# Optimization experiments

Measured on AMD Instinct MI355X. Metric: run time of the kernel, lower is better.

## Reference

```python
import jax, jax.numpy as jnp
import numpy as np

N = 500_000
E = 5_000_000
DIM = 16
LR = 0.005
THRESHOLD = 0.0


def setup_inputs() -> dict:
    key = jax.random.key(0)
    ks = jax.random.split(key, 8)
    s = 1.0 / np.sqrt(DIM)
    return {
        "x": jax.random.normal(ks[0], (N, DIM), jnp.float32),
        "edge_index": jax.random.randint(ks[1], (2, E), 0, N, dtype=jnp.int32),
        "W1": jax.random.normal(ks[2], (DIM, DIM), jnp.float32) * s,
        "b1": jnp.zeros((DIM,), jnp.float32),
        "W2": jax.random.normal(ks[3], (DIM, DIM), jnp.float32) * s,
        "b2": jnp.zeros((DIM,), jnp.float32),
        "W3": jax.random.normal(ks[4], (DIM, DIM), jnp.float32) * s,
        "b3": jnp.zeros((DIM,), jnp.float32),
        "positive": 0,  # negative sample -> nonzero loss branch
    }


def gcn_conv(x, edge_index, W, b):
    # PyG GCNConv: h = x @ W.T, add self-loops, symmetric norm, aggregate at dst.
    n = x.shape[0]
    loop = jnp.arange(n, dtype=edge_index.dtype)
    src = jnp.concatenate([edge_index[0], loop])
    dst = jnp.concatenate([edge_index[1], loop])
    deg = jax.ops.segment_sum(jnp.ones_like(dst, x.dtype), dst, num_segments=n)
    dinv = jnp.where(deg > 0, jax.lax.rsqrt(deg), 0.0)
    norm = dinv[src] * dinv[dst]  # [E+N]
    h = x @ W.T  # [N, out]
    msg = norm[:, None] * h[src]  # irregular gather, memory-bound
    return jax.ops.segment_sum(msg, dst, num_segments=n) + b


def local_loss(g, positive):
    t = THRESHOLD
    if positive:
        return jnp.where(g > t + 10.0, 0.0,
               jnp.where(g < t - 10.0, t - g, jnp.log1p(jnp.exp(t - g))))
    return jnp.where(g > t + 10.0, t + g,
           jnp.where(g < t - 10.0, 0.0, jnp.log1p(jnp.exp(g + t))))


def reference(x, edge_index, W1, b1, W2, b2, W3, b3, positive):
    # Note: the original computes activation_normalizer(x) and loss_derivative(g)
    # into z/driv_loss but immediately overwrites both -> dead code, omitted.
    agg = jnp.float32(0.0)
    Wc, bc = W1, b1  # conv1 params, updated in-place each layer in the original
    x_cur = x
    for (W, b) in ((W1, b1), (W2, b2), (W3, b3)):
        z = jax.nn.relu(gcn_conv(x_cur, edge_index, W, b))
        goodness = jnp.sum(z * z) / z.shape[1]
        agg = agg + local_loss(goodness, positive)
        d = 2.0 * jnp.abs(z)            # activation_gradient(z)
        wd = d * d                      # weighted_deriv
        dW = x_cur.T @ wd               # [in, out]
        db = jnp.sum(wd, axis=0)
        Wc = Wc - LR * dW.T
        bc = bc - LR * db
        x_cur = z
    return agg, Wc, bc
```

## Files before the change

### kernel.cpp

```cpp
#include <hip/hip_runtime.h>
#include <math.h>

#define TPB 256
#define TPB_P 512
#define TPB_A 512
#define LRATE 0.005f

#define LOG_NPB 10
#define NPB (1 << LOG_NPB)
#define CAP 14336

#define LOG_SUP 13
#define NS1 64
#define CAP1 90112
#define NS2 8
#define CHUNK 4096
#define CPT (CHUNK / TPB_P)

#define NTILE 64

#define FXS  65536.0f
#define FXSI (1.0f / 65536.0f)

#if __has_builtin(__builtin_amdgcn_cvt_f32_fp8) && __has_builtin(__builtin_amdgcn_cvt_pk_fp8_f32)
__device__ __forceinline__ float fp8_dec(unsigned char v) {
    return __builtin_amdgcn_cvt_f32_fp8((int)v, 0);
}
__device__ __forceinline__ unsigned fp8_pk4(float a, float b, float c, float d) {
    int w = __builtin_amdgcn_cvt_pk_fp8_f32(a, b, 0, false);
    w = __builtin_amdgcn_cvt_pk_fp8_f32(c, d, w, true);
    return (unsigned)w;
}
#else
__device__ __forceinline__ unsigned char fp8_enc1(float f) {
    unsigned u = __float_as_uint(f);
    unsigned s = (u >> 24) & 0x80u;
    u &= 0x7FFFFFFFu;
    if (u >= 0x43E00000u) return (unsigned char)(s | 0x7E);
    if (u < 0x3C800000u) {
        float a = __uint_as_float(u);
        int m = (int)rintf(a * 512.f);
        return (unsigned char)(s | (unsigned)m);
    }
    unsigned mant = u & 0x7FFFFFu;
    unsigned rest = mant & 0xFFFFFu;
    unsigned keep = u >> 20;
    keep += (rest > 0x80000u || (rest == 0x80000u && (keep & 1u))) ? 1u : 0u;
    int eb = (int)(keep >> 3) - 127 + 7;
    return (unsigned char)(s | (unsigned)((eb << 3) | (int)(keep & 7u)));
}
__device__ __forceinline__ float fp8_dec(unsigned char v) {
    unsigned s = ((unsigned)(v & 0x80u)) << 24;
    unsigned e = (v >> 3) & 0xFu;
    unsigned m = v & 7u;
    if (e == 0) {
        float r = (float)m * 0.001953125f;
        return (v & 0x80u) ? -r : r;
    }
    return __uint_as_float(s | ((e + 120u) << 23) | (m << 20));
}
__device__ __forceinline__ unsigned fp8_pk4(float a, float b, float c, float d) {
    return (unsigned)fp8_enc1(a) | ((unsigned)fp8_enc1(b) << 8) |
           ((unsigned)fp8_enc1(c) << 16) | ((unsigned)fp8_enc1(d) << 24);
}
#endif

#if __has_builtin(__builtin_amdgcn_cvt_pk_f32_fp8)
typedef float __attribute__((ext_vector_type(2))) f32x2;
__device__ __forceinline__ void fp8_dec4(unsigned w, float& a, float& b, float& c, float& d) {
    f32x2 lo = __builtin_amdgcn_cvt_pk_f32_fp8((int)w, false);
    f32x2 hi = __builtin_amdgcn_cvt_pk_f32_fp8((int)w, true);
    a = lo[0]; b = lo[1]; c = hi[0]; d = hi[1];
}
#else
__device__ __forceinline__ void fp8_dec4(unsigned w, float& a, float& b, float& c, float& d) {
    a = fp8_dec((unsigned char)(w & 0xFFu));
    b = fp8_dec((unsigned char)((w >> 8) & 0xFFu));
    c = fp8_dec((unsigned char)((w >> 16) & 0xFFu));
    d = fp8_dec((unsigned char)((w >> 24) & 0xFFu));
}
#endif

__global__ __launch_bounds__(TPB_P) void k_part1(const int* __restrict__ src,
                                                 const int* __restrict__ dst,
                                                 int* __restrict__ bcur1,
                                                 int* __restrict__ grec1,
                                                 int E) {
    __shared__ int hist[NS1], lstart[NS1], lcur[NS1], gbase[NS1];
    __shared__ int lbuf[CHUNK];
    __shared__ unsigned char bbuf[CHUNK];
    int t = threadIdx.x;
    int chunkBase = blockIdx.x * CHUNK;
    if (t < NS1) hist[t] = 0;
    __syncthreads();

    int myb[CPT], myrec[CPT];
#pragma unroll
    for (int k = 0; k < CPT; k++) {
        int e = chunkBase + k * TPB_P + t;
        if (e < E) {
            int d = dst[e];
            int s = src[e];
            myb[k] = d >> LOG_SUP;
            myrec[k] = (s << LOG_SUP) | (d & ((1 << LOG_SUP) - 1));
            atomicAdd(&hist[myb[k]], 1);
        } else myb[k] = -1;
    }
    __syncthreads();
    if (t == 0) {
        int run = 0;
        for (int k2 = 0; k2 < NS1; k2++) {
            int c = hist[k2]; lstart[k2] = run; lcur[k2] = run; run += c;
        }
    }
    __syncthreads();
    if (t < NS1 && hist[t] > 0) gbase[t] = atomicAdd(&bcur1[t * 16], hist[t]);
    __syncthreads();
#pragma unroll
    for (int k = 0; k < CPT; k++) {
        if (myb[k] >= 0) {
            int p = atomicAdd(&lcur[myb[k]], 1);
            lbuf[p] = myrec[k];
            bbuf[p] = (unsigned char)myb[k];
        }
    }
    __syncthreads();
    int total = E - chunkBase; if (total > CHUNK) total = CHUNK;
    for (int p = t; p < total; p += TPB_P) {
        int b = (int)bbuf[p];
        int pos = gbase[b] + (p - lstart[b]);
        if (pos < CAP1) grec1[(size_t)b * CAP1 + pos] = lbuf[p];
    }
}

__global__ __launch_bounds__(TPB_P) void k_part2(const int* __restrict__ bcur1,
                                                 const int* __restrict__ grec1,
                                                 int* __restrict__ bcur,
                                                 int* __restrict__ grec) {
    __shared__ int hist[NS2], lstart[NS2], lcur[NS2], gbase[NS2];
    __shared__ int lbuf[CHUNK];
    __shared__ unsigned char bbuf[CHUNK];
    int t = threadIdx.x;
    int s = blockIdx.x;
    int cnt1 = bcur1[s * 16]; if (cnt1 > CAP1) cnt1 = CAP1;
    int chunkBase = blockIdx.y * CHUNK;
    if (chunkBase >= cnt1) return;
    int total = cnt1 - chunkBase; if (total > CHUNK) total = CHUNK;
    if (t < NS2) hist[t] = 0;
    __syncthreads();

    int myb[CPT], myrec[CPT];
#pragma unroll
    for (int k = 0; k < CPT; k++) {
        int i = chunkBase + k * TPB_P + t;
        if (i < cnt1) {
            int r = grec1[(size_t)s * CAP1 + i];
            int sub = (r >> LOG_NPB) & (NS2 - 1);
            myb[k] = sub;
            myrec[k] = (int)((((unsigned)r) >> LOG_SUP) << LOG_NPB) | (r & (NPB - 1));
            atomicAdd(&hist[sub], 1);
        } else myb[k] = -1;
    }
    __syncthreads();
    if (t == 0) {
        int run = 0;
        for (int k2 = 0; k2 < NS2; k2++) {
            int c = hist[k2]; lstart[k2] = run; lcur[k2] = run; run += c;
        }
    }
    __syncthreads();
    if (t < NS2 && hist[t] > 0) gbase[t] = atomicAdd(&bcur[(s * NS2 + t) * 16], hist[t]);
    __syncthreads();
#pragma unroll
    for (int k = 0; k < CPT; k++) {
        if (myb[k] >= 0) {
            int p = atomicAdd(&lcur[myb[k]], 1);
            lbuf[p] = myrec[k];
            bbuf[p] = (unsigned char)myb[k];
        }
    }
    __syncthreads();
    for (int p = t; p < total; p += TPB_P) {
        int b = (int)bbuf[p];
        int pos = gbase[b] + (p - lstart[b]);
        if (pos < CAP) grec[(size_t)(s * NS2 + b) * CAP + pos] = lbuf[p];
    }
}

__global__ __launch_bounds__(TPB_P) void k_sort(int* __restrict__ bcur,
                                                int* __restrict__ grec,
                                                float* __restrict__ dinv, int N) {
    __shared__ int lbuf[CAP];
    __shared__ int obuf[CAP];
    __shared__ int deg[NPB];
    __shared__ int hist[NTILE];
    __shared__ int curp[NTILE];
    int t = threadIdx.x;
    int b = blockIdx.x;
    int cnt = bcur[b * 16]; if (cnt > CAP) cnt = CAP;
    const size_t base = (size_t)b * CAP;

    for (int i = t; i < NTILE; i += TPB_P) hist[i] = 0;
    for (int i = t; i < NPB; i += TPB_P) deg[i] = 0;
    __syncthreads();
    for (int i = t; i < cnt; i += TPB_P) {
        int r = grec[base + i];
        lbuf[i] = r;
        atomicAdd(&deg[r & (NPB - 1)], 1);
        atomicAdd(&hist[((unsigned)r) >> 23], 1);
    }
    __syncthreads();
    if (t == 0) {
        int run = 0;
#pragma unroll
        for (int k = 0; k < NTILE; k++) { int c = hist[k]; curp[k] = run; run += c; }
    }
    __syncthreads();
    for (int i = t; i < cnt; i += TPB_P) {
        int r = lbuf[i];
        int p = atomicAdd(&curp[((unsigned)r) >> 23], 1);
        obuf[p] = r;
    }
    __syncthreads();
    for (int i = t; i < cnt; i += TPB_P) grec[base + i] = obuf[i];
    int nodeBase = b << LOG_NPB;
    for (int i = t; i < NPB; i += TPB_P) {
        int node = nodeBase + i;
        if (node < N) dinv[node] = rsqrtf((float)(deg[i] + 1));
    }
}

__global__ __launch_bounds__(TPB) void k_h(const float* __restrict__ xc,
                                           const float* __restrict__ W,
                                           const float* __restrict__ dinv,
                                           unsigned* __restrict__ hp, int n) {
    __shared__ float sW[256];
    if (threadIdx.x < 256) sW[threadIdx.x] = W[threadIdx.x];
    __syncthreads();
    int i = blockIdx.x * blockDim.x + threadIdx.x;
    int stride = gridDim.x * blockDim.x;
    for (; i < n; i += stride) {
        float x[16];
        const float4* xr = (const float4*)(xc + (size_t)i * 16);
#pragma unroll
        for (int q = 0; q < 4; q++) {
            float4 v = xr[q];
            x[4*q+0] = v.x; x[4*q+1] = v.y; x[4*q+2] = v.z; x[4*q+3] = v.w;
        }
        float di = dinv[i];
        float hv[16];
#pragma unroll
        for (int j = 0; j < 16; j++) {
            float s = 0.f;
#pragma unroll
            for (int k = 0; k < 16; k++) s = fmaf(x[k], sW[j*16 + k], s);
            hv[j] = di * s;
        }
        uint4 w;
        w.x = fp8_pk4(hv[0],  hv[1],  hv[2],  hv[3]);
        w.y = fp8_pk4(hv[4],  hv[5],  hv[6],  hv[7]);
        w.z = fp8_pk4(hv[8],  hv[9],  hv[10], hv[11]);
        w.w = fp8_pk4(hv[12], hv[13], hv[14], hv[15]);
        ((uint4*)hp)[i] = w;
    }
}

__global__ __launch_bounds__(TPB_A, 4) void k_agg(const int* __restrict__ bcur,
                                                  const int* __restrict__ grec,
                                                  const float* __restrict__ dinv,
                                                  const unsigned* __restrict__ hp32,
                                                  const float* __restrict__ b,
                                                  const float* __restrict__ xc,
                                                  float* __restrict__ z,
                                                  float* __restrict__ partial,
                                                  int nb, int N) {
    __shared__ int accI[16 * NPB];
    int t = threadIdx.x;
    int bkt = blockIdx.x;
    int cnt = bcur[bkt * 16]; if (cnt > CAP) cnt = CAP;
    const int nodeBase = bkt << LOG_NPB;
    const size_t recBase = (size_t)bkt * CAP;

    {
        int4 zv = make_int4(0, 0, 0, 0);
        int4* a4 = (int4*)accI;
        for (int i = t; i < 16 * NPB / 4; i += TPB_A) a4[i] = zv;
    }
    __syncthreads();

    int q = t & 3;
    int gi = t >> 2;
    int j0 = q * 4;
    int base = 0;
    for (; base + 1024 <= cnt; base += 1024) {
        int rec[8];
#pragma unroll
        for (int u = 0; u < 8; u++) rec[u] = grec[recBase + base + u * 128 + gi];
        unsigned w[8];
#pragma unroll
        for (int u = 0; u < 8; u++)
            w[u] = hp32[(size_t)(((unsigned)rec[u]) >> LOG_NPB) * 4 + q];
#pragma unroll
        for (int u = 0; u < 8; u++) {
            int dl = rec[u] & (NPB - 1);
            float f0, f1, f2, f3;
            fp8_dec4(w[u], f0, f1, f2, f3);
            atomicAdd(&accI[(j0 + 0) * NPB + (dl ^ (j0 + 0))], (int)(f0 * FXS));
            atomicAdd(&accI[(j0 + 1) * NPB + (dl ^ (j0 + 1))], (int)(f1 * FXS));
            atomicAdd(&accI[(j0 + 2) * NPB + (dl ^ (j0 + 2))], (int)(f2 * FXS));
            atomicAdd(&accI[(j0 + 3) * NPB + (dl ^ (j0 + 3))], (int)(f3 * FXS));
        }
    }
    for (int e = base + gi; e < cnt; e += 128) {
        int rec = grec[recBase + e];
        unsigned w = hp32[(size_t)(((unsigned)rec) >> LOG_NPB) * 4 + q];
        int dl = rec & (NPB - 1);
        float f0, f1, f2, f3;
        fp8_dec4(w, f0, f1, f2, f3);
        atomicAdd(&accI[(j0 + 0) * NPB + (dl ^ (j0 + 0))], (int)(f0 * FXS));
        atomicAdd(&accI[(j0 + 1) * NPB + (dl ^ (j0 + 1))], (int)(f1 * FXS));
        atomicAdd(&accI[(j0 + 2) * NPB + (dl ^ (j0 + 2))], (int)(f2 * FXS));
        atomicAdd(&accI[(j0 + 3) * NPB + (dl ^ (j0 + 3))], (int)(f3 * FXS));
    }
    __syncthreads();

    const unsigned char* hpB = (const unsigned char*)hp32;
    int j = t & 15;
    int g0 = t >> 4;
    float bj = b[j];
    float accW[16];
#pragma unroll
    for (int k = 0; k < 16; k++) accW[k] = 0.f;
    float accB = 0.f;

    for (int i = g0; i < NPB; i += 32) {
        int node = nodeBase + i;
        if (node >= N) break;
        float sv = fp8_dec(hpB[(size_t)node * 16 + j]);
        float aj = fmaf((float)accI[j * NPB + (i ^ j)], FXSI, sv);
        float zj = fmaxf(fmaf(dinv[node], aj, bj), 0.f);
        z[(size_t)node * 16 + j] = zj;
        float wdj = 4.f * zj * zj;
        accB += wdj;
        const float4* xrow = (const float4*)(xc + (size_t)node * 16);
        float4 x0 = xrow[0], x1 = xrow[1], x2 = xrow[2], x3 = xrow[3];
        accW[0]  = fmaf(x0.x, wdj, accW[0]);  accW[1]  = fmaf(x0.y, wdj, accW[1]);
        accW[2]  = fmaf(x0.z, wdj, accW[2]);  accW[3]  = fmaf(x0.w, wdj, accW[3]);
        accW[4]  = fmaf(x1.x, wdj, accW[4]);  accW[5]  = fmaf(x1.y, wdj, accW[5]);
        accW[6]  = fmaf(x1.z, wdj, accW[6]);  accW[7]  = fmaf(x1.w, wdj, accW[7]);
        accW[8]  = fmaf(x2.x, wdj, accW[8]);  accW[9]  = fmaf(x2.y, wdj, accW[9]);
        accW[10] = fmaf(x2.z, wdj, accW[10]); accW[11] = fmaf(x2.w, wdj, accW[11]);
        accW[12] = fmaf(x3.x, wdj, accW[12]); accW[13] = fmaf(x3.y, wdj, accW[13]);
        accW[14] = fmaf(x3.z, wdj, accW[14]); accW[15] = fmaf(x3.w, wdj, accW[15]);
    }
    __syncthreads();

    float (*red)[17] = (float (*)[17])accI;
#pragma unroll
    for (int k = 0; k < 16; k++) red[t][k] = accW[k];
    red[t][16] = accB;
    __syncthreads();
    if (t < 256) {
        int kk = t >> 4;
        int jj = t & 15;
        float s = 0.f;
#pragma unroll
        for (int g = 0; g < 32; g++) s += red[g * 16 + jj][kk];
        partial[(size_t)(kk * 16 + jj) * nb + bkt] = s;
    }
    if (t < 16) {
        float sb = 0.f;
#pragma unroll
        for (int g = 0; g < 32; g++) sb += red[g * 16 + t][16];
        partial[(size_t)(256 + t) * nb + bkt] = sb;
    }
}

__global__ __launch_bounds__(TPB) void k_reduce(const float* __restrict__ partial,
                                                float* __restrict__ acc,
                                                int nb, int total) {
    int wid = (blockIdx.x * blockDim.x + threadIdx.x) >> 6;
    int lane = threadIdx.x & 63;
    if (wid >= total) return;
    const float* p = partial + (size_t)wid * nb;
    float s = 0.f;
    for (int b = lane; b < nb; b += 64) s += p[b];
#pragma unroll
    for (int off = 32; off > 0; off >>= 1) s += __shfl_down(s, off, 64);
    if (lane == 0) acc[wid] = s;
}

__device__ __forceinline__ float local_loss_f(float g, int positive) {
    const float t = 0.0f;
    if (positive) {
        if (g > t + 10.f) return 0.f;
        if (g < t - 10.f) return t - g;
        return log1pf(expf(t - g));
    } else {
        if (g > t + 10.f) return t + g;
        if (g < t - 10.f) return 0.f;
        return log1pf(expf(g + t));
    }
}

__global__ void k_final(const float* __restrict__ W1, const float* __restrict__ b1,
                        const float* __restrict__ acc, const int* __restrict__ positive,
                        float* __restrict__ outv) {
    int t = threadIdx.x;
    if (t < 256) {
        int jj = t >> 4, kk = t & 15;
        float s = 0.f;
#pragma unroll
        for (int l = 0; l < 3; l++) s += acc[l * 272 + kk * 16 + jj];
        outv[1 + t] = W1[t] - LRATE * s;
    }
    if (t < 16) {
        float s = 0.f;
#pragma unroll
        for (int l = 0; l < 3; l++) s += acc[l * 272 + 256 + t];
        outv[257 + t] = b1[t] - LRATE * s;
    }
    if (t == 0) {
        int pos = positive[0];
        float agg = 0.f;
#pragma unroll
        for (int l = 0; l < 3; l++) {
            float g = 0.f;
#pragma unroll
            for (int jj = 0; jj < 16; jj++) g += acc[l * 272 + 256 + jj];
            g *= (1.0f / 64.0f);
            agg += local_loss_f(g, pos);
        }
        outv[0] = agg;
    }
}

extern "C" void kernel_launch(void* const* d_in, const int* in_sizes, int n_in,
                              void* d_out, int out_size, void* d_ws, size_t ws_size,
                              hipStream_t stream) {
    const float* x  = (const float*)d_in[0];
    const int*   ei = (const int*)d_in[1];
    const float* W1 = (const float*)d_in[2];
    const float* b1 = (const float*)d_in[3];
    const float* W2 = (const float*)d_in[4];
    const float* b2 = (const float*)d_in[5];
    const float* W3 = (const float*)d_in[6];
    const float* b3 = (const float*)d_in[7];
    const int* positive = (const int*)d_in[8];
    float* outv = (float*)d_out;

    const int N = in_sizes[0] / 16;
    const int E = in_sizes[1] / 2;
    const int nbuck = (N + NPB - 1) >> LOG_NPB;
    const int nsuper = (N + (1 << LOG_SUP) - 1) >> LOG_SUP;
    const int nbpad = nsuper * NS2;

    char* ws = (char*)d_ws;
    size_t off = 0;
    auto carve = [&](size_t bytes) -> void* {
        void* p = ws + off;
        off = (off + bytes + 255) & ~(size_t)255;
        return p;
    };
    int*   bcur   = (int*)  carve((size_t)(nbpad + NS1) * 16 * 4);
    int*   bcur1  = bcur + (size_t)nbpad * 16;
    int*   grec   = (int*)  carve((size_t)nbpad * CAP * 4);
    float* dinv   = (float*)carve((size_t)N * 4);
    float* acc    = (float*)carve(3 * 272 * 4);
    float* part   = (float*)carve((size_t)3 * 272 * nbuck * 4);
    unsigned* hp  = (unsigned*)carve((size_t)N * 16);
    float* P1     = (float*)carve((size_t)N * 64);
    float* P2     = (float*)carve((size_t)N * 64);
    int*   grec1  = (int*)P2;

    hipMemsetAsync(bcur, 0, (size_t)(nbpad + NS1) * 16 * 4, stream);

    const int* src = ei;
    const int* dst = ei + E;

    int p1Blocks = (E + CHUNK - 1) / CHUNK;
    k_part1<<<p1Blocks, TPB_P, 0, stream>>>(src, dst, bcur1, grec1, E);
    dim3 g2(nsuper, CAP1 / CHUNK);
    k_part2<<<g2, TPB_P, 0, stream>>>(bcur1, grec1, bcur, grec);
    k_sort<<<nbuck, TPB_P, 0, stream>>>(bcur, grec, dinv, N);

    const float* Ws[3] = {W1, W2, W3};
    const float* bss[3] = {b1, b2, b3};
    float* outs[3] = {P1, P2, P1};

    int nodeBlocks = (N + TPB - 1) / TPB;

    const float* xc = x;
    for (int l = 0; l < 3; l++) {
        k_h<<<nodeBlocks, TPB, 0, stream>>>(xc, Ws[l], dinv, hp, N);
        k_agg<<<nbuck, TPB_A, 0, stream>>>(bcur, grec, dinv, hp, bss[l],
                                           xc, outs[l],
                                           part + (size_t)l * 272 * nbuck, nbuck, N);
        xc = outs[l];
    }
    int totalElems = 3 * 272;
    k_reduce<<<(totalElems * 64 + TPB - 1) / TPB, TPB, 0, stream>>>(part, acc, nbuck, totalElems);
    k_final<<<1, 256, 0, stream>>>(W1, b1, acc, positive, outv);
}
```

Measured before the change: 396.6 us.

## Pack two biased fixed-point channels per 64-bit LDS atomic and fuse final reduction

The aggregation kernel now accumulates two feature channels per 64-bit shared-memory atomic. Each 32-bit lane gets a positive bias so carries cannot cross between halves, and the bias is removed afterwards using the node degree recovered from dinv. This halves the number of LDS atomics per edge; the batch unroll is also cut from 8 to 4. The separate reduce kernel and final kernel are merged into one single-block kernel, saving a launch but running the cross-bucket reduction on only 13 wavefronts. The degree recovery via rintf(1/dinv^2) and bias overflow bounds carry correctness risk.

```diff
diff --git a/kernel.cpp b/kernel.cpp
--- a/kernel.cpp
+++ b/kernel.cpp
@@ -21,6 +21,7 @@
 
 #define FXS  65536.0f
 #define FXSI (1.0f / 65536.0f)
+#define FXBIAS (1 << 20)
 
 #if __has_builtin(__builtin_amdgcn_cvt_f32_fp8) && __has_builtin(__builtin_amdgcn_cvt_pk_fp8_f32)
 __device__ __forceinline__ float fp8_dec(unsigned char v) {
@@ -80,6 +81,12 @@
     d = fp8_dec((unsigned char)((w >> 24) & 0xFFu));
 }
 #endif
+
+__device__ __forceinline__ unsigned long long pack2(float f0, float f1) {
+    unsigned lo = (unsigned)(FXBIAS + (int)(f0 * FXS));
+    unsigned hi = (unsigned)(FXBIAS + (int)(f1 * FXS));
+    return (unsigned long long)lo | ((unsigned long long)hi << 32);
+}
 
 __global__ __launch_bounds__(TPB_P) void k_part1(const int* __restrict__ src,
                                                  const int* __restrict__ dst,
@@ -274,41 +281,36 @@
                                                   float* __restrict__ z,
                                                   float* __restrict__ partial,
                                                   int nb, int N) {
-    __shared__ int accI[16 * NPB];
+    __shared__ unsigned long long accP[8 * NPB];
     int t = threadIdx.x;
     int bkt = blockIdx.x;
     int cnt = bcur[bkt * 16]; if (cnt > CAP) cnt = CAP;
     const int nodeBase = bkt << LOG_NPB;
     const size_t recBase = (size_t)bkt * CAP;
 
-    {
-        int4 zv = make_int4(0, 0, 0, 0);
-        int4* a4 = (int4*)accI;
-        for (int i = t; i < 16 * NPB / 4; i += TPB_A) a4[i] = zv;
-    }
+    for (int i = t; i < 8 * NPB; i += TPB_A) accP[i] = 0ull;
     __syncthreads();
 
     int q = t & 3;
     int gi = t >> 2;
-    int j0 = q * 4;
+    int p0 = q * 2;
+    int p1 = q * 2 + 1;
     int base = 0;
-    for (; base + 1024 <= cnt; base += 1024) {
-        int rec[8];
-#pragma unroll
-        for (int u = 0; u < 8; u++) rec[u] = grec[recBase + base + u * 128 + gi];
-        unsigned w[8];
-#pragma unroll
-        for (int u = 0; u < 8; u++)
+    for (; base + 512 <= cnt; base += 512) {
+        int rec[4];
+#pragma unroll
+        for (int u = 0; u < 4; u++) rec[u] = grec[recBase + base + u * 128 + gi];
+        unsigned w[4];
+#pragma unroll
+        for (int u = 0; u < 4; u++)
             w[u] = hp32[(size_t)(((unsigned)rec[u]) >> LOG_NPB) * 4 + q];
 #pragma unroll
-        for (int u = 0; u < 8; u++) {
+        for (int u = 0; u < 4; u++) {
             int dl = rec[u] & (NPB - 1);
             float f0, f1, f2, f3;
             fp8_dec4(w[u], f0, f1, f2, f3);
-            atomicAdd(&accI[(j0 + 0) * NPB + (dl ^ (j0 + 0))], (int)(f0 * FXS));
-            atomicAdd(&accI[(j0 + 1) * NPB + (dl ^ (j0 + 1))], (int)(f1 * FXS));
-            atomicAdd(&accI[(j0 + 2) * NPB + (dl ^ (j0 + 2))], (int)(f2 * FXS));
-            atomicAdd(&accI[(j0 + 3) * NPB + (dl ^ (j0 + 3))], (int)(f3 * FXS));
+            atomicAdd(&accP[p0 * NPB + (dl ^ p0)], pack2(f0, f1));
+            atomicAdd(&accP[p1 * NPB + (dl ^ p1)], pack2(f2, f3));
         }
     }
     for (int e = base + gi; e < cnt; e += 128) {
@@ -317,16 +319,17 @@
         int dl = rec & (NPB - 1);
         float f0, f1, f2, f3;
         fp8_dec4(w, f0, f1, f2, f3);
-        atomicAdd(&accI[(j0 + 0) * NPB + (dl ^ (j0 + 0))], (int)(f0 * FXS));
-        atomicAdd(&accI[(j0 + 1) * NPB + (dl ^ (j0 + 1))], (int)(f1 * FXS));
-        atomicAdd(&accI[(j0 + 2) * NPB + (dl ^ (j0 + 2))], (int)(f2 * FXS));
-        atomicAdd(&accI[(j0 + 3) * NPB + (dl ^ (j0 + 3))], (int)(f3 * FXS));
+        atomicAdd(&accP[p0 * NPB + (dl ^ p0)], pack2(f0, f1));
+        atomicAdd(&accP[p1 * NPB + (dl ^ p1)], pack2(f2, f3));
     }
     __syncthreads();
 
     const unsigned char* hpB = (const unsigned char*)hp32;
+    const int* accI32 = (const int*)accP;
     int j = t & 15;
     int g0 = t >> 4;
+    int pj = j >> 1;
+    int hj = j & 1;
     float bj = b[j];
     float accW[16];
 #pragma unroll
@@ -336,9 +339,13 @@
     for (int i = g0; i < NPB; i += 32) {
         int node = nodeBase + i;
         if (node >= N) break;
+        float di = dinv[node];
+        int cdeg = (int)rintf(1.0f / (di * di)) - 1;
+        int raw = accI32[(pj * NPB + (i ^ pj)) * 2 + hj];
+        int ai = raw - cdeg * FXBIAS;
         float sv = fp8_dec(hpB[(size_t)node * 16 + j]);
-        float aj = fmaf((float)accI[j * NPB + (i ^ j)], FXSI, sv);
-        float zj = fmaxf(fmaf(dinv[node], aj, bj), 0.f);
+        float aj = fmaf((float)ai, FXSI, sv);
+        float zj = fmaxf(fmaf(di, aj, bj), 0.f);
         z[(size_t)node * 16 + j] = zj;
         float wdj = 4.f * zj * zj;
         accB += wdj;
@@ -355,7 +362,7 @@
     }
     __syncthreads();
 
-    float (*red)[17] = (float (*)[17])accI;
+    float (*red)[17] = (float (*)[17])accP;
 #pragma unroll
     for (int k = 0; k < 16; k++) red[t][k] = accW[k];
     red[t][16] = accB;
@@ -374,20 +381,6 @@
         for (int g = 0; g < 32; g++) sb += red[g * 16 + t][16];
         partial[(size_t)(256 + t) * nb + bkt] = sb;
     }
-}
-
-__global__ __launch_bounds__(TPB) void k_reduce(const float* __restrict__ partial,
-                                                float* __restrict__ acc,
-                                                int nb, int total) {
-    int wid = (blockIdx.x * blockDim.x + threadIdx.x) >> 6;
-    int lane = threadIdx.x & 63;
-    if (wid >= total) return;
-    const float* p = partial + (size_t)wid * nb;
-    float s = 0.f;
-    for (int b = lane; b < nb; b += 64) s += p[b];
-#pragma unroll
-    for (int off = 32; off > 0; off >>= 1) s += __shfl_down(s, off, 64);
-    if (lane == 0) acc[wid] = s;
 }
 
 __device__ __forceinline__ float local_loss_f(float g, int positive) {
@@ -403,21 +396,34 @@
     }
 }
 
-__global__ void k_final(const float* __restrict__ W1, const float* __restrict__ b1,
-                        const float* __restrict__ acc, const int* __restrict__ positive,
-                        float* __restrict__ outv) {
+__global__ __launch_bounds__(832) void k_fin(const float* __restrict__ W1,
+                                             const float* __restrict__ b1,
+                                             const float* __restrict__ partial,
+                                             const int* __restrict__ positive,
+                                             float* __restrict__ outv, int nb) {
+    __shared__ float accL[3 * 272];
     int t = threadIdx.x;
+    int wid = t >> 6, lane = t & 63;
+    for (int e = wid; e < 3 * 272; e += 13) {
+        const float* p = partial + (size_t)e * nb;
+        float s = 0.f;
+        for (int b = lane; b < nb; b += 64) s += p[b];
+#pragma unroll
+        for (int off = 32; off > 0; off >>= 1) s += __shfl_down(s, off, 64);
+        if (lane == 0) accL[e] = s;
+    }
+    __syncthreads();
     if (t < 256) {
         int jj = t >> 4, kk = t & 15;
         float s = 0.f;
 #pragma unroll
-        for (int l = 0; l < 3; l++) s += acc[l * 272 + kk * 16 + jj];
+        for (int l = 0; l < 3; l++) s += accL[l * 272 + kk * 16 + jj];
         outv[1 + t] = W1[t] - LRATE * s;
     }
     if (t < 16) {
         float s = 0.f;
 #pragma unroll
-        for (int l = 0; l < 3; l++) s += acc[l * 272 + 256 + t];
+        for (int l = 0; l < 3; l++) s += accL[l * 272 + 256 + t];
         outv[257 + t] = b1[t] - LRATE * s;
     }
     if (t == 0) {
@@ -427,7 +433,7 @@
         for (int l = 0; l < 3; l++) {
             float g = 0.f;
 #pragma unroll
-            for (int jj = 0; jj < 16; jj++) g += acc[l * 272 + 256 + jj];
+            for (int jj = 0; jj < 16; jj++) g += accL[l * 272 + 256 + jj];
             g *= (1.0f / 64.0f);
             agg += local_loss_f(g, pos);
         }
@@ -466,7 +472,6 @@
     int*   bcur1  = bcur + (size_t)nbpad * 16;
     int*   grec   = (int*)  carve((size_t)nbpad * CAP * 4);
     float* dinv   = (float*)carve((size_t)N * 4);
-    float* acc    = (float*)carve(3 * 272 * 4);
     float* part   = (float*)carve((size_t)3 * 272 * nbuck * 4);
     unsigned* hp  = (unsigned*)carve((size_t)N * 16);
     float* P1     = (float*)carve((size_t)N * 64);
@@ -498,7 +503,5 @@
                                            part + (size_t)l * 272 * nbuck, nbuck, N);
         xc = outs[l];
     }
-    int totalElems = 3 * 272;
-    k_reduce<<<(totalElems * 64 + TPB - 1) / TPB, TPB, 0, stream>>>(part, acc, nbuck, totalElems);
-    k_final<<<1, 256, 0, stream>>>(W1, b1, acc, positive, outv);
-}
+    k_fin<<<1, 832, 0, stream>>>(W1, b1, part, positive, outv, nbuck);
+}
```

New measurement: 540.2 us. 36.2% more time.
